# Kernel tuning notes

Measured on AMD Instinct MI355X. Metric: run time of the kernel, lower is better.

Reference implementation:

```python
import jax, jax.numpy as jnp
import numpy as np

N_HEADS = 16
LN_EPS = 1e-5


def _layer_norm(x, g, b):
    mu = jnp.mean(x, axis=-1, keepdims=True)
    var = jnp.mean(jnp.square(x - mu), axis=-1, keepdims=True)
    return (x - mu) * jax.lax.rsqrt(var + LN_EPS) * g + b


def setup_inputs() -> dict:
    key = jax.random.key(0)
    ks = jax.random.split(key, 6)
    B, S, D = 2, 2048, 1024
    d_ff = 4 * D
    sc = lambda fan_in: 1.0 / np.sqrt(fan_in)
    return {
        "x": jax.random.normal(ks[0], (B, S, D), jnp.float32),
        "in_proj_w": jax.random.normal(ks[1], (3 * D, D), jnp.float32) * sc(D),
        "in_proj_b": jnp.zeros((3 * D,), jnp.float32),
        "out_proj_w": jax.random.normal(ks[2], (D, D), jnp.float32) * sc(D),
        "out_proj_b": jnp.zeros((D,), jnp.float32),
        "ln1_g": jnp.ones((D,), jnp.float32),
        "ln1_b": jnp.zeros((D,), jnp.float32),
        "w1": jax.random.normal(ks[3], (d_ff, D), jnp.float32) * sc(D),
        "b1": jnp.zeros((d_ff,), jnp.float32),
        "w2": jax.random.normal(ks[4], (D, d_ff), jnp.float32) * sc(d_ff),
        "b2": jnp.zeros((D,), jnp.float32),
        "ln2_g": jnp.ones((D,), jnp.float32),
        "ln2_b": jnp.zeros((D,), jnp.float32),
        "window": 128,
    }


def reference(x, in_proj_w, in_proj_b, out_proj_w, out_proj_b,
              ln1_g, ln1_b, w1, b1, w2, b2, ln2_g, ln2_b, window):
    B, S, D = x.shape
    H = N_HEADS
    hd = D // H

    # fused QKV projection (torch Linear convention: x @ W.T + b)
    qkv = x @ in_proj_w.T + in_proj_b            # (B, S, 3D)
    q, k, v = jnp.split(qkv, 3, axis=-1)
    to_heads = lambda t: t.reshape(B, S, H, hd).transpose(0, 2, 1, 3)  # (B,H,S,hd)
    q, k, v = to_heads(q), to_heads(k), to_heads(v)

    scores = jnp.einsum("bhqd,bhkd->bhqk", q, k) / jnp.sqrt(jnp.asarray(hd, x.dtype))
    # banded mask: position i attends to j with |i - j| <= window
    idx = jnp.arange(S)
    band = jnp.abs(idx[:, None] - idx[None, :]) <= window   # (S, S) bool
    scores = jnp.where(band, scores, -jnp.inf)
    probs = jax.nn.softmax(scores, axis=-1)

    attn = jnp.einsum("bhqk,bhkd->bhqd", probs, v)           # (B,H,S,hd)
    attn = attn.transpose(0, 2, 1, 3).reshape(B, S, D)
    attn_out = attn @ out_proj_w.T + out_proj_b

    x2 = _layer_norm(x + attn_out, ln1_g, ln1_b)
    ff = jax.nn.relu(x2 @ w1.T + b1) @ w2.T + b2
    x3 = _layer_norm(x2 + ff, ln2_g, ln2_b)
    return x3
```

## Files before the change

### kernel.cpp

```cpp
#include <hip/hip_runtime.h>
#include <hip/hip_bf16.h>

#define AS1 __attribute__((address_space(1)))
#define AS3 __attribute__((address_space(3)))

typedef __bf16 bf16x8_t __attribute__((ext_vector_type(8)));
typedef float f32x4_t __attribute__((ext_vector_type(4)));
typedef unsigned short ushort_t;
typedef unsigned int uint_t;

static __device__ __forceinline__ ushort_t f2b(float f) {
    __hip_bfloat16 h = __float2bfloat16(f);
    return __builtin_bit_cast(unsigned short, h);
}

__global__ __launch_bounds__(256) void cast_f32_bf16(const float* __restrict__ in,
                                                     ushort_t* __restrict__ out, int n4) {
    int i = blockIdx.x * 256 + threadIdx.x;
    if (i < n4) {
        float4 v = ((const float4*)in)[i];
        ushort4 o;
        o.x = f2b(v.x); o.y = f2b(v.y); o.z = f2b(v.z); o.w = f2b(v.w);
        ((ushort4*)out)[i] = o;
    }
}

#define EPI_BIAS 1
#define EPI_RELU 2
#define EPI_RES  4
#define EPI_OUTF 8
#define EPI_OUTB 16

template <int F>
__global__ __launch_bounds__(256, 2) void gemm_bt(const ushort_t* __restrict__ A,
                                                  const ushort_t* __restrict__ B,
                                                  const float* __restrict__ bias,
                                                  const float* __restrict__ res,
                                                  float* __restrict__ outf,
                                                  ushort_t* __restrict__ outb,
                                                  int M, int N, int K) {
    __shared__ ushort_t la[128 * 32];
    __shared__ ushort_t lb[128 * 32];
    const int t = threadIdx.x;
    const int n0 = blockIdx.x * 128;
    const int m0 = blockIdx.y * 128;
    const int lane = t & 63;
    const int w = t >> 6;
    const int wr = w >> 1, wc = w & 1;
    const int r16 = lane & 15, kq = lane >> 4;

    const int srow = t >> 2;
    const int scg = t & 3;

    f32x4_t acc[4][4] = {};

    const size_t arow0 = (size_t)(m0 + srow) * K + scg * 8;
    const size_t brow0 = (size_t)(n0 + srow) * K + scg * 8;

    for (int k0 = 0; k0 < K; k0 += 32) {
#pragma unroll
        for (int p = 0; p < 2; ++p) {
            const ushort_t* ga = A + arow0 + (size_t)p * 64 * K + k0;
            const ushort_t* gb = B + brow0 + (size_t)p * 64 * K + k0;
            __builtin_amdgcn_global_load_lds((AS1 void*)ga, (AS3 void*)(la + (t + 256 * p) * 8), 16, 0, 0);
            __builtin_amdgcn_global_load_lds((AS1 void*)gb, (AS3 void*)(lb + (t + 256 * p) * 8), 16, 0, 0);
        }
        __syncthreads();
        bf16x8_t af[4], bfr[4];
#pragma unroll
        for (int mi = 0; mi < 4; ++mi)
            af[mi] = *(const bf16x8_t*)(la + (wr * 64 + mi * 16 + r16) * 32 + kq * 8);
#pragma unroll
        for (int ni = 0; ni < 4; ++ni)
            bfr[ni] = *(const bf16x8_t*)(lb + (wc * 64 + ni * 16 + r16) * 32 + kq * 8);
#pragma unroll
        for (int mi = 0; mi < 4; ++mi)
#pragma unroll
            for (int ni = 0; ni < 4; ++ni)
                acc[mi][ni] = __builtin_amdgcn_mfma_f32_16x16x32_bf16(af[mi], bfr[ni], acc[mi][ni], 0, 0, 0);
        __syncthreads();
    }

#pragma unroll
    for (int mi = 0; mi < 4; ++mi) {
#pragma unroll
        for (int ni = 0; ni < 4; ++ni) {
            const int row = m0 + wr * 64 + mi * 16 + kq * 4;
            const int col = n0 + wc * 64 + ni * 16 + r16;
            float bv = (F & EPI_BIAS) ? bias[col] : 0.f;
#pragma unroll
            for (int i = 0; i < 4; ++i) {
                float v = acc[mi][ni][i] + bv;
                const size_t off = (size_t)(row + i) * N + col;
                if (F & EPI_RES) v += res[off];
                if (F & EPI_RELU) v = fmaxf(v, 0.f);
                if (F & EPI_OUTF) outf[off] = v;
                if (F & EPI_OUTB) outb[off] = f2b(v);
            }
        }
    }
}

__global__ __launch_bounds__(256, 4) void flash_mfma(const ushort_t* __restrict__ qkv,
                                                     ushort_t* __restrict__ attn) {
    const int S = 2048;
    const int h = blockIdx.y, bb = blockIdx.z;
    const int q0 = blockIdx.x * 64;
    const int t = threadIdx.x;
    const int w = t >> 6, lane = t & 63;
    const int r16 = lane & 15, g = lane >> 4;

    __shared__ ushort_t lk[64 * 72];
    __shared__ ushort_t lv[64 * 68];
    __shared__ ushort_t lp[4 * 16 * 72];

    const ushort_t* base = qkv + (size_t)bb * S * 3072 + (size_t)h * 64;

    bf16x8_t qa[2];
    {
        const ushort_t* qrow = base + (size_t)(q0 + 16 * w + r16) * 3072;
        qa[0] = *(const bf16x8_t*)(qrow + g * 8);
        qa[1] = *(const bf16x8_t*)(qrow + 32 + g * 8);
    }

    f32x4_t O[4] = {};
    float mrow[4] = {-1e30f, -1e30f, -1e30f, -1e30f};
    float lrow[4] = {0.f, 0.f, 0.f, 0.f};

    for (int it = 0; it < 5; ++it) {
        const int kt0 = q0 - 128 + 64 * it;
        if (kt0 < 0 || kt0 >= S) continue;

#pragma unroll
        for (int pass = 0; pass < 2; ++pass) {
            const int c = t + 256 * pass;
            const int key = c >> 3, dc = c & 7;
            const ushort_t* src = base + (size_t)(kt0 + key) * 3072 + dc * 8;
            uint4 kk = *(const uint4*)(src + 1024);
            uint4 vv = *(const uint4*)(src + 2048);
            *(uint4*)(lk + key * 72 + dc * 8) = kk;
            uint2* vd = (uint2*)(lv + key * 68 + dc * 8);
            vd[0] = make_uint2(vv.x, vv.y);
            vd[1] = make_uint2(vv.z, vv.w);
        }
        __syncthreads();

        f32x4_t s[4];
#pragma unroll
        for (int sub = 0; sub < 4; ++sub) {
            const ushort_t* krow = lk + (16 * sub + r16) * 72;
            bf16x8_t kb0 = *(const bf16x8_t*)(krow + g * 8);
            bf16x8_t kb1 = *(const bf16x8_t*)(krow + 32 + g * 8);
            f32x4_t z = {};
            z = __builtin_amdgcn_mfma_f32_16x16x32_bf16(qa[0], kb0, z, 0, 0, 0);
            z = __builtin_amdgcn_mfma_f32_16x16x32_bf16(qa[1], kb1, z, 0, 0, 0);
            s[sub] = z;
        }

        float alpha[4];
#pragma unroll
        for (int reg = 0; reg < 4; ++reg) {
            const int i = q0 + 16 * w + g * 4 + reg;
            float rm = -1e30f;
#pragma unroll
            for (int sub = 0; sub < 4; ++sub) {
                const int j = kt0 + 16 * sub + r16;
                const int d = i - j;
                const bool valid = (d <= 128) && (d >= -128);
                float v = valid ? s[sub][reg] * 0.125f : -1e30f;
                s[sub][reg] = v;
                rm = fmaxf(rm, v);
            }
#pragma unroll
            for (int msk = 1; msk < 16; msk <<= 1) rm = fmaxf(rm, __shfl_xor(rm, msk));
            const float mnew = fmaxf(mrow[reg], rm);
            alpha[reg] = __expf(mrow[reg] - mnew);
            mrow[reg] = mnew;
            float rs = 0.f;
#pragma unroll
            for (int sub = 0; sub < 4; ++sub) {
                float p = __expf(s[sub][reg] - mnew);
                s[sub][reg] = p;
                rs += p;
            }
#pragma unroll
            for (int msk = 1; msk < 16; msk <<= 1) rs += __shfl_xor(rs, msk);
            lrow[reg] = lrow[reg] * alpha[reg] + rs;
#pragma unroll
            for (int dd = 0; dd < 4; ++dd) O[dd][reg] *= alpha[reg];
        }

        ushort_t* pw = lp + w * 16 * 72;
#pragma unroll
        for (int sub = 0; sub < 4; ++sub)
#pragma unroll
            for (int reg = 0; reg < 4; ++reg)
                pw[(g * 4 + reg) * 72 + 16 * sub + r16] = f2b(s[sub][reg]);

        bf16x8_t pa0 = *(const bf16x8_t*)(pw + r16 * 72 + g * 8);
        bf16x8_t pa1 = *(const bf16x8_t*)(pw + r16 * 72 + 32 + g * 8);
        const __bf16* lvb = (const __bf16*)lv;
#pragma unroll
        for (int dd = 0; dd < 4; ++dd) {
            bf16x8_t vb0, vb1;
#pragma unroll
            for (int j = 0; j < 8; ++j) {
                vb0[j] = lvb[(g * 8 + j) * 68 + dd * 16 + r16];
                vb1[j] = lvb[(32 + g * 8 + j) * 68 + dd * 16 + r16];
            }
            O[dd] = __builtin_amdgcn_mfma_f32_16x16x32_bf16(pa0, vb0, O[dd], 0, 0, 0);
            O[dd] = __builtin_amdgcn_mfma_f32_16x16x32_bf16(pa1, vb1, O[dd], 0, 0, 0);
        }
        __syncthreads();
    }

#pragma unroll
    for (int reg = 0; reg < 4; ++reg) {
        const float inv = 1.0f / lrow[reg];
        const int i = q0 + 16 * w + g * 4 + reg;
        ushort_t* orow = attn + ((size_t)(bb * S + i)) * 1024 + (size_t)h * 64;
#pragma unroll
        for (int dd = 0; dd < 4; ++dd)
            orow[dd * 16 + r16] = f2b(O[dd][reg] * inv);
    }
}

__global__ __launch_bounds__(256) void layernorm_k(const float* __restrict__ in,
                                                   const float* __restrict__ g,
                                                   const float* __restrict__ bta,
                                                   float* __restrict__ outf,
                                                   ushort_t* __restrict__ outb) {
    const int row = blockIdx.x;
    const int t = threadIdx.x;
    const float4 v = ((const float4*)(in + (size_t)row * 1024))[t];
    float s = v.x + v.y + v.z + v.w;
    float s2 = v.x * v.x + v.y * v.y + v.z * v.z + v.w * v.w;
#pragma unroll
    for (int off = 32; off > 0; off >>= 1) {
        s += __shfl_down(s, off);
        s2 += __shfl_down(s2, off);
    }
    __shared__ float red[8];
    const int w = t >> 6, lane = t & 63;
    if (lane == 0) { red[w] = s; red[4 + w] = s2; }
    __syncthreads();
    float S1 = red[0] + red[1] + red[2] + red[3];
    float S2 = red[4] + red[5] + red[6] + red[7];
    float mean = S1 * (1.f / 1024.f);
    float var = S2 * (1.f / 1024.f) - mean * mean;
    float r = rsqrtf(var + 1e-5f);
    float4 gg = ((const float4*)g)[t];
    float4 bb = ((const float4*)bta)[t];
    float4 o;
    o.x = (v.x - mean) * r * gg.x + bb.x;
    o.y = (v.y - mean) * r * gg.y + bb.y;
    o.z = (v.z - mean) * r * gg.z + bb.z;
    o.w = (v.w - mean) * r * gg.w + bb.w;
    ((float4*)(outf + (size_t)row * 1024))[t] = o;
    if (outb) {
        ushort4 ob;
        ob.x = f2b(o.x); ob.y = f2b(o.y); ob.z = f2b(o.z); ob.w = f2b(o.w);
        ((ushort4*)(outb + (size_t)row * 1024))[t] = ob;
    }
}

extern "C" void kernel_launch(void* const* d_in, const int* in_sizes, int n_in,
                              void* d_out, int out_size, void* d_ws, size_t ws_size,
                              hipStream_t stream) {
    const float* x          = (const float*)d_in[0];
    const float* in_proj_w  = (const float*)d_in[1];
    const float* in_proj_b  = (const float*)d_in[2];
    const float* out_proj_w = (const float*)d_in[3];
    const float* out_proj_b = (const float*)d_in[4];
    const float* ln1_g      = (const float*)d_in[5];
    const float* ln1_b      = (const float*)d_in[6];
    const float* w1         = (const float*)d_in[7];
    const float* b1         = (const float*)d_in[8];
    const float* w2         = (const float*)d_in[9];
    const float* b2         = (const float*)d_in[10];
    const float* ln2_g      = (const float*)d_in[11];
    const float* ln2_b      = (const float*)d_in[12];

    char* ws = (char*)d_ws;
    ushort_t* xb    = (ushort_t*)(ws + (0ull << 20));
    ushort_t* wqkvb = (ushort_t*)(ws + (8ull << 20));
    ushort_t* woutb = (ushort_t*)(ws + (14ull << 20));
    ushort_t* w1b   = (ushort_t*)(ws + (16ull << 20));
    ushort_t* w2b   = (ushort_t*)(ws + (24ull << 20));
    ushort_t* qkvb  = (ushort_t*)(ws + (32ull << 20));
    ushort_t* attnb = (ushort_t*)(ws + (56ull << 20));
    float*    y1    = (float*)(ws + (64ull << 20));
    float*    x2f   = (float*)(ws + (80ull << 20));
    ushort_t* x2b   = (ushort_t*)(ws + (96ull << 20));
    ushort_t* hb    = (ushort_t*)(ws + (104ull << 20));
    (void)in_sizes; (void)n_in; (void)out_size; (void)ws_size;

    cast_f32_bf16<<<4096, 256, 0, stream>>>(x, xb, 1048576);
    cast_f32_bf16<<<3072, 256, 0, stream>>>(in_proj_w, wqkvb, 786432);
    cast_f32_bf16<<<1024, 256, 0, stream>>>(out_proj_w, woutb, 262144);
    cast_f32_bf16<<<4096, 256, 0, stream>>>(w1, w1b, 1048576);
    cast_f32_bf16<<<4096, 256, 0, stream>>>(w2, w2b, 1048576);

    gemm_bt<EPI_BIAS | EPI_OUTB><<<dim3(24, 32), 256, 0, stream>>>(
        xb, wqkvb, in_proj_b, nullptr, nullptr, qkvb, 4096, 3072, 1024);

    flash_mfma<<<dim3(32, 16, 2), 256, 0, stream>>>(qkvb, attnb);

    gemm_bt<EPI_BIAS | EPI_RES | EPI_OUTF><<<dim3(8, 32), 256, 0, stream>>>(
        attnb, woutb, out_proj_b, x, y1, nullptr, 4096, 1024, 1024);

    layernorm_k<<<4096, 256, 0, stream>>>(y1, ln1_g, ln1_b, x2f, x2b);

    gemm_bt<EPI_BIAS | EPI_RELU | EPI_OUTB><<<dim3(32, 32), 256, 0, stream>>>(
        x2b, w1b, b1, nullptr, nullptr, hb, 4096, 4096, 1024);

    gemm_bt<EPI_BIAS | EPI_RES | EPI_OUTF><<<dim3(8, 32), 256, 0, stream>>>(
        hb, w2b, b2, x2f, y1, nullptr, 4096, 1024, 4096);

    layernorm_k<<<4096, 256, 0, stream>>>(y1, ln2_g, ln2_b, (float*)d_out, nullptr);
}
```

Baseline: 357.9 us.

## Split-K the narrow GEMMs, fuse reduction into layernorm, batch weight casts

```diff
diff --git a/kernel.cpp b/kernel.cpp
--- a/kernel.cpp
+++ b/kernel.cpp
@@ -14,36 +14,46 @@
     return __builtin_bit_cast(unsigned short, h);
 }
 
-__global__ __launch_bounds__(256) void cast_f32_bf16(const float* __restrict__ in,
-                                                     ushort_t* __restrict__ out, int n4) {
-    int i = blockIdx.x * 256 + threadIdx.x;
-    if (i < n4) {
-        float4 v = ((const float4*)in)[i];
-        ushort4 o;
-        o.x = f2b(v.x); o.y = f2b(v.y); o.z = f2b(v.z); o.w = f2b(v.w);
-        ((ushort4*)out)[i] = o;
-    }
+struct CastArgs {
+    const float* src[5];
+    ushort_t* dst[5];
+    int cum[6];
+};
+
+__global__ __launch_bounds__(256) void cast_all(CastArgs a) {
+    const int i = blockIdx.x * 256 + threadIdx.x;
+    if (i >= a.cum[5]) return;
+    int s = 0;
+#pragma unroll
+    for (int k = 1; k < 5; ++k) s += (i >= a.cum[k]);
+    const int idx = i - a.cum[s];
+    float4 v = ((const float4*)a.src[s])[idx];
+    ushort4 o;
+    o.x = f2b(v.x); o.y = f2b(v.y); o.z = f2b(v.z); o.w = f2b(v.w);
+    ((ushort4*)a.dst[s])[idx] = o;
 }
 
 #define EPI_BIAS 1
 #define EPI_RELU 2
-#define EPI_RES  4
 #define EPI_OUTF 8
 #define EPI_OUTB 16
+
+struct P4 { float* p[4]; };
 
 template <int F>
 __global__ __launch_bounds__(256, 2) void gemm_bt(const ushort_t* __restrict__ A,
                                                   const ushort_t* __restrict__ B,
                                                   const float* __restrict__ bias,
-                                                  const float* __restrict__ res,
-                                                  float* __restrict__ outf,
+                                                  P4 outs,
                                                   ushort_t* __restrict__ outb,
-                                                  int M, int N, int K) {
+                                                  int M, int N, int Kc, int ld) {
     __shared__ ushort_t la[128 * 32];
     __shared__ ushort_t lb[128 * 32];
     const int t = threadIdx.x;
     const int n0 = blockIdx.x * 128;
     const int m0 = blockIdx.y * 128;
+    const int z = blockIdx.z;
+    const int k0 = z * Kc;
     const int lane = t & 63;
     const int w = t >> 6;
     const int wr = w >> 1, wc = w & 1;
@@ -54,14 +64,14 @@
 
     f32x4_t acc[4][4] = {};
 
-    const size_t arow0 = (size_t)(m0 + srow) * K + scg * 8;
-    const size_t brow0 = (size_t)(n0 + srow) * K + scg * 8;
-
-    for (int k0 = 0; k0 < K; k0 += 32) {
+    const size_t arow0 = (size_t)(m0 + srow) * ld + scg * 8 + k0;
+    const size_t brow0 = (size_t)(n0 + srow) * ld + scg * 8 + k0;
+
+    for (int kk = 0; kk < Kc; kk += 32) {
 #pragma unroll
         for (int p = 0; p < 2; ++p) {
-            const ushort_t* ga = A + arow0 + (size_t)p * 64 * K + k0;
-            const ushort_t* gb = B + brow0 + (size_t)p * 64 * K + k0;
+            const ushort_t* ga = A + arow0 + (size_t)p * 64 * ld + kk;
+            const ushort_t* gb = B + brow0 + (size_t)p * 64 * ld + kk;
             __builtin_amdgcn_global_load_lds((AS1 void*)ga, (AS3 void*)(la + (t + 256 * p) * 8), 16, 0, 0);
             __builtin_amdgcn_global_load_lds((AS1 void*)gb, (AS3 void*)(lb + (t + 256 * p) * 8), 16, 0, 0);
         }
@@ -81,6 +91,7 @@
         __syncthreads();
     }
 
+    float* outf = outs.p[z];
 #pragma unroll
     for (int mi = 0; mi < 4; ++mi) {
 #pragma unroll
@@ -92,7 +103,6 @@
             for (int i = 0; i < 4; ++i) {
                 float v = acc[mi][ni][i] + bv;
                 const size_t off = (size_t)(row + i) * N + col;
-                if (F & EPI_RES) v += res[off];
                 if (F & EPI_RELU) v = fmaxf(v, 0.f);
                 if (F & EPI_OUTF) outf[off] = v;
                 if (F & EPI_OUTB) outb[off] = f2b(v);
@@ -225,14 +235,36 @@
     }
 }
 
-__global__ __launch_bounds__(256) void layernorm_k(const float* __restrict__ in,
-                                                   const float* __restrict__ g,
-                                                   const float* __restrict__ bta,
-                                                   float* __restrict__ outf,
-                                                   ushort_t* __restrict__ outb) {
+template <int NP>
+__global__ __launch_bounds__(256) void ln_red(const float* __restrict__ p0,
+                                              const float* __restrict__ p1,
+                                              const float* __restrict__ p2,
+                                              const float* __restrict__ p3,
+                                              const float* __restrict__ bias,
+                                              const float* __restrict__ res,
+                                              const float* __restrict__ g,
+                                              const float* __restrict__ bta,
+                                              float* __restrict__ outf,
+                                              ushort_t* __restrict__ outb) {
     const int row = blockIdx.x;
     const int t = threadIdx.x;
-    const float4 v = ((const float4*)(in + (size_t)row * 1024))[t];
+    const size_t idx = (size_t)row * 256 + t;
+    float4 v = ((const float4*)p0)[idx];
+    {
+        float4 a = ((const float4*)p1)[idx];
+        v.x += a.x; v.y += a.y; v.z += a.z; v.w += a.w;
+    }
+    if (NP == 4) {
+        float4 a = ((const float4*)p2)[idx];
+        float4 b = ((const float4*)p3)[idx];
+        v.x += a.x + b.x; v.y += a.y + b.y; v.z += a.z + b.z; v.w += a.w + b.w;
+    }
+    {
+        float4 bb = ((const float4*)bias)[t];
+        float4 rr = ((const float4*)res)[idx];
+        v.x += bb.x + rr.x; v.y += bb.y + rr.y; v.z += bb.z + rr.z; v.w += bb.w + rr.w;
+    }
+
     float s = v.x + v.y + v.z + v.w;
     float s2 = v.x * v.x + v.y * v.y + v.z * v.z + v.w * v.w;
 #pragma unroll
@@ -256,11 +288,11 @@
     o.y = (v.y - mean) * r * gg.y + bb.y;
     o.z = (v.z - mean) * r * gg.z + bb.z;
     o.w = (v.w - mean) * r * gg.w + bb.w;
-    ((float4*)(outf + (size_t)row * 1024))[t] = o;
+    ((float4*)outf)[idx] = o;
     if (outb) {
         ushort4 ob;
         ob.x = f2b(o.x); ob.y = f2b(o.y); ob.z = f2b(o.z); ob.w = f2b(o.w);
-        ((ushort4*)(outb + (size_t)row * 1024))[t] = ob;
+        ((ushort4*)outb)[idx] = ob;
     }
 }
 
@@ -293,29 +325,47 @@
     float*    x2f   = (float*)(ws + (80ull << 20));
     ushort_t* x2b   = (ushort_t*)(ws + (96ull << 20));
     ushort_t* hb    = (ushort_t*)(ws + (104ull << 20));
+    float* op_p1  = (float*)(ws + (32ull << 20));
+    float* f2_p1  = (float*)(ws + (0ull << 20));
+    float* f2_p2  = (float*)(ws + (32ull << 20));
+    float* f2_p3  = (float*)(ws + (48ull << 20));
     (void)in_sizes; (void)n_in; (void)out_size; (void)ws_size;
 
-    cast_f32_bf16<<<4096, 256, 0, stream>>>(x, xb, 1048576);
-    cast_f32_bf16<<<3072, 256, 0, stream>>>(in_proj_w, wqkvb, 786432);
-    cast_f32_bf16<<<1024, 256, 0, stream>>>(out_proj_w, woutb, 262144);
-    cast_f32_bf16<<<4096, 256, 0, stream>>>(w1, w1b, 1048576);
-    cast_f32_bf16<<<4096, 256, 0, stream>>>(w2, w2b, 1048576);
-
-    gemm_bt<EPI_BIAS | EPI_OUTB><<<dim3(24, 32), 256, 0, stream>>>(
-        xb, wqkvb, in_proj_b, nullptr, nullptr, qkvb, 4096, 3072, 1024);
+    CastArgs ca;
+    ca.src[0] = x;  ca.dst[0] = xb;
+    ca.src[1] = in_proj_w;  ca.dst[1] = wqkvb;
+    ca.src[2] = out_proj_w; ca.dst[2] = woutb;
+    ca.src[3] = w1; ca.dst[3] = w1b;
+    ca.src[4] = w2; ca.dst[4] = w2b;
+    ca.cum[0] = 0;
+    ca.cum[1] = 1048576;
+    ca.cum[2] = 1048576 + 786432;
+    ca.cum[3] = 1048576 + 786432 + 262144;
+    ca.cum[4] = 1048576 + 786432 + 262144 + 1048576;
+    ca.cum[5] = 1048576 + 786432 + 262144 + 1048576 + 1048576;
+    cast_all<<<(ca.cum[5] + 255) / 256, 256, 0, stream>>>(ca);
+
+    P4 none = {{nullptr, nullptr, nullptr, nullptr}};
+
+    gemm_bt<EPI_BIAS | EPI_OUTB><<<dim3(24, 32, 1), 256, 0, stream>>>(
+        xb, wqkvb, in_proj_b, none, qkvb, 4096, 3072, 1024, 1024);
 
     flash_mfma<<<dim3(32, 16, 2), 256, 0, stream>>>(qkvb, attnb);
 
-    gemm_bt<EPI_BIAS | EPI_RES | EPI_OUTF><<<dim3(8, 32), 256, 0, stream>>>(
-        attnb, woutb, out_proj_b, x, y1, nullptr, 4096, 1024, 1024);
-
-    layernorm_k<<<4096, 256, 0, stream>>>(y1, ln1_g, ln1_b, x2f, x2b);
-
-    gemm_bt<EPI_BIAS | EPI_RELU | EPI_OUTB><<<dim3(32, 32), 256, 0, stream>>>(
-        x2b, w1b, b1, nullptr, nullptr, hb, 4096, 4096, 1024);
-
-    gemm_bt<EPI_BIAS | EPI_RES | EPI_OUTF><<<dim3(8, 32), 256, 0, stream>>>(
-        hb, w2b, b2, x2f, y1, nullptr, 4096, 1024, 4096);
-
-    layernorm_k<<<4096, 256, 0, stream>>>(y1, ln2_g, ln2_b, (float*)d_out, nullptr);
-}
+    P4 op = {{y1, op_p1, nullptr, nullptr}};
+    gemm_bt<EPI_OUTF><<<dim3(8, 32, 2), 256, 0, stream>>>(
+        attnb, woutb, nullptr, op, nullptr, 4096, 1024, 512, 1024);
+
+    ln_red<2><<<4096, 256, 0, stream>>>(y1, op_p1, nullptr, nullptr,
+                                        out_proj_b, x, ln1_g, ln1_b, x2f, x2b);
+
+    gemm_bt<EPI_BIAS | EPI_RELU | EPI_OUTB><<<dim3(32, 32, 1), 256, 0, stream>>>(
+        x2b, w1b, b1, none, hb, 4096, 4096, 1024, 1024);
+
+    P4 f2 = {{y1, f2_p1, f2_p2, f2_p3}};
+    gemm_bt<EPI_OUTF><<<dim3(8, 32, 4), 256, 0, stream>>>(
+        hb, w2b, nullptr, f2, nullptr, 4096, 1024, 1024, 4096);
+
+    ln_red<4><<<4096, 256, 0, stream>>>(y1, f2_p1, f2_p2, f2_p3,
+                                        b2, x2f, ln2_g, ln2_b, (float*)d_out, nullptr);
+}
```

Measured after the change: 337.2 us. 5.8% less time.
